# Performance work log

Measured on AMD Instinct MI355X. Metric: run time of the kernel, lower is better.

The kernel has to match this reference:

```python
import jax, jax.numpy as jnp
import numpy as np
from jax.ops import segment_sum

N_NODES = 100000
IN_CH = 128
HIDDEN = 256
N_EDGES = 1600000


def setup_inputs() -> dict:
    key = jax.random.key(0)
    ks = jax.random.split(key, 8)
    x = jax.random.normal(ks[0], (N_NODES, IN_CH), dtype=jnp.float32)
    edge_index = jax.random.randint(ks[1], (2, N_EDGES), 0, N_NODES, dtype=jnp.int64)
    edges = jax.random.randint(ks[2], (N_EDGES, 2), 0, N_NODES, dtype=jnp.int64)
    s1 = 1.0 / np.sqrt(IN_CH)
    s2 = 1.0 / np.sqrt(HIDDEN)
    W1l = jax.random.normal(ks[3], (IN_CH, HIDDEN), dtype=jnp.float32) * s1
    W1r = jax.random.normal(ks[4], (IN_CH, HIDDEN), dtype=jnp.float32) * s1
    b1 = jnp.zeros((HIDDEN,), dtype=jnp.float32)
    W2l = jax.random.normal(ks[5], (HIDDEN, HIDDEN), dtype=jnp.float32) * s2
    W2r = jax.random.normal(ks[6], (HIDDEN, HIDDEN), dtype=jnp.float32) * s2
    b2 = jnp.zeros((HIDDEN,), dtype=jnp.float32)
    return {"x": x, "edge_index": edge_index, "edges": edges,
            "W1l": W1l, "b1": b1, "W1r": W1r,
            "W2l": W2l, "b2": b2, "W2r": W2r}


def _sage_conv(x, src, dst, Wl, b, Wr, n_nodes):
    # PyG SAGEConv (aggr='mean'): out = lin_l(mean_{j in N(i)} x_j) + lin_r(x_i)
    msg_sum = segment_sum(x[src], dst, num_segments=n_nodes)        # [N, F]
    deg = segment_sum(jnp.ones((src.shape[0],), x.dtype), dst, num_segments=n_nodes)
    mean = msg_sum / jnp.maximum(deg, 1.0)[:, None]                 # zero-deg -> 0
    return mean @ Wl + b + x @ Wr


def reference(x, edge_index, edges, W1l, b1, W1r, W2l, b2, W2r):
    src, dst = edge_index[0], edge_index[1]
    n = x.shape[0]
    h = jax.nn.relu(_sage_conv(x, src, dst, W1l, b1, W1r, n))
    z = _sage_conv(h, src, dst, W2l, b2, W2r, n)                    # [N, hidden]
    # decode: dot product over candidate edge pairs
    return jnp.sum(z[edges[:, 0]] * z[edges[:, 1]], axis=-1)        # [E2]
```

## Files before the change

### kernel.cpp

```cpp
#include <hip/hip_runtime.h>

#define IN_CH 128
#define HID   256
#define PB_VT 16
#define BCAP  6144

typedef __attribute__((ext_vector_type(8))) short bf16x8;
typedef __attribute__((ext_vector_type(4))) float f32x4;
typedef __attribute__((ext_vector_type(2))) float f32x2;
typedef __attribute__((ext_vector_type(8))) unsigned short ushort8;

__device__ __forceinline__ ushort f2b(float f) {
    unsigned u = __float_as_uint(f);
    unsigned r = (u + 0x7fffu + ((u >> 16) & 1u)) >> 16;
    return (ushort)r;
}
__device__ __forceinline__ float b2f(ushort h) {
    return __uint_as_float(((unsigned)h) << 16);
}
__device__ __forceinline__ void fp8x8_to_f32(uint2 v, float f[8]) {
    f32x2 a = __builtin_amdgcn_cvt_pk_f32_fp8((int)v.x, false);
    f32x2 b = __builtin_amdgcn_cvt_pk_f32_fp8((int)v.x, true);
    f32x2 c = __builtin_amdgcn_cvt_pk_f32_fp8((int)v.y, false);
    f32x2 d = __builtin_amdgcn_cvt_pk_f32_fp8((int)v.y, true);
    f[0] = a[0]; f[1] = a[1]; f[2] = b[0]; f[3] = b[1];
    f[4] = c[0]; f[5] = c[1]; f[6] = d[0]; f[7] = d[1];
}

__device__ __forceinline__ void prep_w_body(const float* __restrict__ Wl,
                                            const float* __restrict__ Wr,
                                            ushort* __restrict__ Wt,
                                            int KH, bool permK, int idx) {
    int ktot = 2 * KH;
    if (idx >= 256 * ktot) return;
    int n = idx / ktot, k = idx % ktot;
    int kh = (k < KH) ? k : (k - KH);
    int c = kh;
    if (permK) {
        int j = kh & 63;
        c = (kh & ~63) | ((j & 3) * 16 + (j >> 2));
    }
    float v = (k < KH) ? Wl[(size_t)c * 256 + n] : Wr[(size_t)c * 256 + n];
    Wt[idx] = f2b(v);
}

__global__ __launch_bounds__(256)
void fused_cvt_prep(const float* __restrict__ x, ushort* __restrict__ xb, int n4, int nCvt,
                    const float* __restrict__ W1l, const float* __restrict__ W1r, ushort* __restrict__ Wt1,
                    const float* __restrict__ W2l, const float* __restrict__ W2r, ushort* __restrict__ Wt2,
                    int* __restrict__ bucketCntG, int* __restrict__ bucketCntP) {
    int b = blockIdx.x;
    int t = threadIdx.x;
    if (b < nCvt) {
        int i = b * 256 + t;
        if (i < n4) {
            float4 v = ((const float4*)x)[i];
            ushort4 u;
            u.x = f2b(v.x); u.y = f2b(v.y); u.z = f2b(v.z); u.w = f2b(v.w);
            ((ushort4*)xb)[i] = u;
        }
    } else if (b < nCvt + 256) {
        prep_w_body(W1l, W1r, Wt1, IN_CH, false, (b - nCvt) * 256 + t);
    } else if (b < nCvt + 256 + 512) {
        prep_w_body(W2l, W2r, Wt2, HID, true, (b - nCvt - 256) * 256 + t);
    } else {
        bucketCntG[t] = 0;
        bucketCntG[t + 256] = 0;
        bucketCntP[t] = 0;
        bucketCntP[t + 256] = 0;
    }
}

__global__ __launch_bounds__(256)
void scatter_reserve_kernel(const int* __restrict__ src, const int* __restrict__ dst,
                            const int* __restrict__ edges,
                            int* __restrict__ bucketCntG, int* __restrict__ bucketCntP,
                            unsigned* __restrict__ tmpG, unsigned long long* __restrict__ tmpP,
                            int E, int E2, int NBUK, int NBG) {
    __shared__ int hist[512];
    __shared__ int cur[512];
    int t = threadIdx.x;
    bool isG = (int)blockIdx.x < NBG;
    int blk = isG ? blockIdx.x : blockIdx.x - NBG;
    for (int i = t; i < NBUK; i += 256) hist[i] = 0;
    __syncthreads();
    long long e0 = (long long)blk * (256 * PB_VT);
    if (isG) {
#pragma unroll
        for (int i = 0; i < PB_VT; i++) {
            long long e = e0 + i * 256 + t;
            if (e < E) atomicAdd(&hist[dst[e] >> 8], 1);
        }
    } else {
#pragma unroll
        for (int i = 0; i < PB_VT; i++) {
            long long e = e0 + i * 256 + t;
            if (e < E2) atomicAdd(&hist[edges[e * 2] >> 8], 1);
        }
    }
    __syncthreads();
    int* bcnt = isG ? bucketCntG : bucketCntP;
    for (int i = t; i < NBUK; i += 256) {
        int hc = hist[i];
        cur[i] = (hc > 0) ? atomicAdd(&bcnt[i], hc) : 0;
    }
    __syncthreads();
    if (isG) {
#pragma unroll
        for (int i = 0; i < PB_VT; i++) {
            long long e = e0 + i * 256 + t;
            if (e < E) {
                int d = dst[e];
                int bk = d >> 8;
                int pos = atomicAdd(&cur[bk], 1);
                tmpG[(size_t)bk * BCAP + pos] = ((unsigned)src[e] << 8) | (unsigned)(d & 255);
            }
        }
    } else {
#pragma unroll
        for (int i = 0; i < PB_VT; i++) {
            long long e = e0 + i * 256 + t;
            if (e < E2) {
                int2 ab = *(const int2*)(edges + e * 2);
                int bk = ab.x >> 8;
                int pos = atomicAdd(&cur[bk], 1);
                tmpP[(size_t)bk * BCAP + pos] = ((unsigned long long)(unsigned)(ab.x & 255) << 56)
                                              | ((unsigned long long)(unsigned)ab.y << 32)
                                              | (unsigned)e;
            }
        }
    }
}

__global__ __launch_bounds__(256)
void bucket_sort_kernel(const unsigned* __restrict__ tmpG, const unsigned long long* __restrict__ tmpP,
                        const int* __restrict__ bucketCntG, const int* __restrict__ bucketCntP,
                        int* __restrict__ count, int* __restrict__ offs,
                        int* __restrict__ nbr, unsigned long long* __restrict__ pairs,
                        int N, int Npad, int NBUK) {
    __shared__ int h[256], loffs[256], lcur[256];
    int t = threadIdx.x;
    bool isG = (int)blockIdx.x < NBUK;
    int b = isG ? blockIdx.x : blockIdx.x - NBUK;
    int s = b * BCAP;
    int c = isG ? bucketCntG[b] : bucketCntP[b];
    h[t] = 0;
    __syncthreads();
    if (isG) {
        for (int i = t; i < c; i += 256) atomicAdd(&h[tmpG[s + i] & 255], 1);
    } else {
        for (int i = t; i < c; i += 256) atomicAdd(&h[(int)(tmpP[s + i] >> 56)], 1);
    }
    __syncthreads();
    int v = h[t];
    loffs[t] = v;
    __syncthreads();
    for (int d = 1; d < 256; d <<= 1) {
        int u = (t >= d) ? loffs[t - d] : 0;
        __syncthreads(); loffs[t] += u; __syncthreads();
    }
    int excl = loffs[t] - v;
    lcur[t] = excl;
    int node = b * 256 + t;
    if (node < N) {
        int base = isG ? 0 : Npad;
        count[base + node] = v;
        offs[base + node] = s + excl;
    }
    __syncthreads();
    if (isG) {
        for (int i = t; i < c; i += 256) {
            unsigned w = tmpG[s + i];
            int p = atomicAdd(&lcur[w & 255], 1);
            nbr[s + p] = (int)(w >> 8);
        }
    } else {
        for (int i = t; i < c; i += 256) {
            unsigned long long w = tmpP[s + i];
            int p = atomicAdd(&lcur[(int)(w >> 56)], 1);
            pairs[s + p] = w & 0x00FFFFFFFFFFFFFFull;
        }
    }
}

__global__ void agg1_kernel(const ushort* __restrict__ xb, const int* __restrict__ nbr,
                            const int* __restrict__ offs, const int* __restrict__ count,
                            ushort* __restrict__ agg, int N) {
    int w = blockIdx.x * 4 + (threadIdx.x >> 6);
    if (w >= N) return;
    int lane = threadIdx.x & 63;
    int grp = lane >> 4, gl = lane & 15;
    int start = offs[w], cnt = count[w];
    float a0[8], a1[8];
#pragma unroll
    for (int i = 0; i < 8; i++) { a0[i] = 0.0f; a1[i] = 0.0f; }
    int j = grp;
    for (; j + 4 < cnt; j += 8) {
        int s0 = nbr[start + j];
        int s1 = nbr[start + j + 4];
        ushort8 v0 = *(const ushort8*)(xb + (size_t)s0 * IN_CH + gl * 8);
        ushort8 v1 = *(const ushort8*)(xb + (size_t)s1 * IN_CH + gl * 8);
#pragma unroll
        for (int i = 0; i < 8; i++) { a0[i] += b2f(v0[i]); a1[i] += b2f(v1[i]); }
    }
    if (j < cnt) {
        int s0 = nbr[start + j];
        ushort8 v0 = *(const ushort8*)(xb + (size_t)s0 * IN_CH + gl * 8);
#pragma unroll
        for (int i = 0; i < 8; i++) a0[i] += b2f(v0[i]);
    }
#pragma unroll
    for (int i = 0; i < 8; i++) {
        a0[i] += a1[i];
        a0[i] += __shfl_xor(a0[i], 16, 64);
        a0[i] += __shfl_xor(a0[i], 32, 64);
    }
    if (grp == 0) {
        float r = 1.0f / fmaxf((float)cnt, 1.0f);
        ushort8 o;
#pragma unroll
        for (int i = 0; i < 8; i++) o[i] = f2b(a0[i] * r);
        *(ushort8*)(agg + (size_t)w * IN_CH + gl * 8) = o;
    }
}

__global__ void agg2_kernel(const unsigned char* __restrict__ h8, const int* __restrict__ nbr,
                            const int* __restrict__ offs, const int* __restrict__ count,
                            ushort* __restrict__ agg, int N) {
    int w = blockIdx.x * 4 + (threadIdx.x >> 6);
    if (w >= N) return;
    int lane = threadIdx.x & 63;
    int half = lane >> 5, hl = lane & 31;
    int start = offs[w], cnt = count[w];
    float a0[8], a1[8];
#pragma unroll
    for (int i = 0; i < 8; i++) { a0[i] = 0.0f; a1[i] = 0.0f; }
    int j = half;
    for (; j + 6 < cnt; j += 8) {
        int s0 = nbr[start + j];
        int s1 = nbr[start + j + 2];
        int s2 = nbr[start + j + 4];
        int s3 = nbr[start + j + 6];
        uint2 v0 = *(const uint2*)(h8 + (size_t)s0 * HID + hl * 8);
        uint2 v1 = *(const uint2*)(h8 + (size_t)s1 * HID + hl * 8);
        uint2 v2 = *(const uint2*)(h8 + (size_t)s2 * HID + hl * 8);
        uint2 v3 = *(const uint2*)(h8 + (size_t)s3 * HID + hl * 8);
        float f0[8], f1[8], f2[8], f3[8];
        fp8x8_to_f32(v0, f0); fp8x8_to_f32(v1, f1);
        fp8x8_to_f32(v2, f2); fp8x8_to_f32(v3, f3);
#pragma unroll
        for (int i = 0; i < 8; i++) {
            a0[i] += f0[i] + f2[i];
            a1[i] += f1[i] + f3[i];
        }
    }
    for (; j < cnt; j += 2) {
        int s0 = nbr[start + j];
        uint2 v0 = *(const uint2*)(h8 + (size_t)s0 * HID + hl * 8);
        float f0[8];
        fp8x8_to_f32(v0, f0);
#pragma unroll
        for (int i = 0; i < 8; i++) a0[i] += f0[i];
    }
#pragma unroll
    for (int i = 0; i < 8; i++) {
        a0[i] += a1[i];
        a0[i] += __shfl_xor(a0[i], 32, 64);
    }
    if (half == 0) {
        float r = 1.0f / fmaxf((float)cnt, 1.0f);
        ushort8 o;
#pragma unroll
        for (int i = 0; i < 8; i++) o[i] = f2b(a0[i] * r);
        *(ushort8*)(agg + (size_t)w * HID + hl * 8) = o;
    }
}

template<int KTOT, bool RELU, bool WBF16, bool WFP8>
__global__ __launch_bounds__(512, 4)
void sage_gemm_mfma(const ushort* __restrict__ Aleft, const ushort* __restrict__ Aright,
                    const ushort* __restrict__ Wt, const float* __restrict__ bias,
                    ushort* __restrict__ out, unsigned char* __restrict__ out8, int N) {
    constexpr int KH = KTOT / 2;
    __shared__ ushort smem[2048 + 8192];
    ushort* As = smem;
    ushort* Bs = smem + 2048;

    const int t = threadIdx.x;
    const int wave = t >> 6;
    const int lane = t & 63;
    const int quad = lane >> 4;
    const int l16  = lane & 15;
    const int rowBase = blockIdx.x * 64;

    const int aRow = t >> 3;
    const int aK   = (t & 7) * 4;
    const bool aRowOK = (rowBase + aRow) < N;
    const int aLds = ((aRow >> 4) * 64 + (aRow & 15) * 4 + (aK >> 3)) * 8 + (aK & 7);

    const int bN   = t >> 1;
    const int bCh0 = (t & 1) * 2;
    const int bFragBase = (bN >> 6) * 256 + ((bN >> 4) & 3) * 64 + (bN & 15) * 4;

    int bFrag[2];
#pragma unroll
    for (int nt = 0; nt < 2; nt++) {
        int c = wave * 32 + nt * 16 + l16;
        bFrag[nt] = ((c >> 6) * 256 + ((c >> 4) & 3) * 64 + (c & 15) * 4 + quad) * 8;
    }

    f32x4 acc[4][2];
#pragma unroll
    for (int i = 0; i < 4; i++)
#pragma unroll
        for (int j = 0; j < 2; j++) acc[i][j] = (f32x4)0.0f;

    unsigned long long aReg = 0ull;
    ulonglong2 bReg[2];
    if (aRowOK)
        aReg = *(const unsigned long long*)(Aleft + (size_t)(rowBase + aRow) * KH + aK);
    bReg[0] = *(const ulonglong2*)(Wt + (size_t)bN * KTOT + bCh0 * 8);
    bReg[1] = *(const ulonglong2*)(Wt + (size_t)bN * KTOT + (bCh0 + 1) * 8);

    for (int k0 = 0; k0 < KTOT; k0 += 32) {
        __syncthreads();
        *(unsigned long long*)&As[aLds] = aReg;
        *(ulonglong2*)&Bs[(bFragBase + bCh0) * 8]     = bReg[0];
        *(ulonglong2*)&Bs[(bFragBase + bCh0 + 1) * 8] = bReg[1];

        int kn = k0 + 32;
        if (kn < KTOT) {
            if (aRowOK) {
                const ushort* Ap = (kn < KH)
                    ? (Aleft  + (size_t)(rowBase + aRow) * KH + (kn + aK))
                    : (Aright + (size_t)(rowBase + aRow) * KH + (kn - KH + aK));
                aReg = *(const unsigned long long*)Ap;
            }
            bReg[0] = *(const ulonglong2*)(Wt + (size_t)bN * KTOT + kn + bCh0 * 8);
            bReg[1] = *(const ulonglong2*)(Wt + (size_t)bN * KTOT + kn + (bCh0 + 1) * 8);
        }
        __syncthreads();

        bf16x8 af[4], bf[2];
#pragma unroll
        for (int mt = 0; mt < 4; mt++)
            af[mt] = *(const bf16x8*)&As[(mt * 64 + l16 * 4 + quad) * 8];
#pragma unroll
        for (int nt = 0; nt < 2; nt++)
            bf[nt] = *(const bf16x8*)&Bs[bFrag[nt]];
#pragma unroll
        for (int mt = 0; mt < 4; mt++)
#pragma unroll
            for (int nt = 0; nt < 2; nt++)
                acc[mt][nt] = __builtin_amdgcn_mfma_f32_16x16x32_bf16(
                    af[mt], bf[nt], acc[mt][nt], 0, 0, 0);
    }

    float bv[2];
#pragma unroll
    for (int nt = 0; nt < 2; nt++) bv[nt] = bias[wave * 32 + nt * 16 + l16];
    ushort* tile = smem;

#pragma unroll
    for (int hf = 0; hf < 2; hf++) {
        __syncthreads();
#pragma unroll
        for (int mh = 0; mh < 2; mh++) {
            int mt = hf * 2 + mh;
#pragma unroll
            for (int reg = 0; reg < 4; reg++) {
                int rl = mh * 16 + quad * 4 + reg;
                float v0 = acc[mt][0][reg] + bv[0];
                float v1 = acc[mt][1][reg] + bv[1];
                if (RELU) { v0 = fmaxf(v0, 0.0f); v1 = fmaxf(v1, 0.0f); }
                ushort2 o;
                o.x = f2b(v0); o.y = f2b(v1);
                *(ushort2*)&tile[rl * 256 + (wave >> 1) * 64 + l16 * 4 + (wave & 1) * 2] = o;
            }
        }
        __syncthreads();
#pragma unroll
        for (int i = 0; i < 2; i++) {
            int ch = i * 512 + t;
            int rl = ch >> 5, c16 = ch & 31;
            int row = rowBase + hf * 32 + rl;
            if (row < N) {
                ushort8 w = *(const ushort8*)&tile[rl * 256 + c16 * 8];
                if (WBF16)
                    *(ushort8*)(out + (size_t)row * 256 + c16 * 8) = w;
                if (WFP8) {
                    int u0 = __builtin_amdgcn_cvt_pk_fp8_f32(b2f(w[0]), b2f(w[1]), 0, false);
                    u0 = __builtin_amdgcn_cvt_pk_fp8_f32(b2f(w[2]), b2f(w[3]), u0, true);
                    int u1 = __builtin_amdgcn_cvt_pk_fp8_f32(b2f(w[4]), b2f(w[5]), 0, false);
                    u1 = __builtin_amdgcn_cvt_pk_fp8_f32(b2f(w[6]), b2f(w[7]), u1, true);
                    uint2 o8;
                    o8.x = (unsigned)u0; o8.y = (unsigned)u1;
                    *(uint2*)(out8 + (size_t)row * 256 + c16 * 8) = o8;
                }
            }
        }
    }
}

__global__ void decode2_kernel(const unsigned char* __restrict__ z8,
                               const unsigned long long* __restrict__ pairs,
                               const int* __restrict__ offsA, const int* __restrict__ countA,
                               float* __restrict__ out, int N) {
    int a = blockIdx.x * 4 + (threadIdx.x >> 6);
    if (a >= N) return;
    int cnt = countA[a];
    if (cnt == 0) return;
    int lane = threadIdx.x & 63;
    int half = lane >> 5, hl = lane & 31;
    int start = offsA[a];

    float ar[8];
    {
        uint2 va = *(const uint2*)(z8 + (size_t)a * HID + hl * 8);
        fp8x8_to_f32(va, ar);
    }

    int j = half;
    for (; j + 6 < cnt; j += 8) {
        unsigned long long p0 = pairs[start + j];
        unsigned long long p1 = pairs[start + j + 2];
        unsigned long long p2 = pairs[start + j + 4];
        unsigned long long p3 = pairs[start + j + 6];
        int b0 = (int)((p0 >> 32) & 0xFFFFFFu), e0 = (int)(p0 & 0xffffffffu);
        int b1 = (int)((p1 >> 32) & 0xFFFFFFu), e1 = (int)(p1 & 0xffffffffu);
        int b2 = (int)((p2 >> 32) & 0xFFFFFFu), e2 = (int)(p2 & 0xffffffffu);
        int b3 = (int)((p3 >> 32) & 0xFFFFFFu), e3 = (int)(p3 & 0xffffffffu);
        uint2 v0 = *(const uint2*)(z8 + (size_t)b0 * HID + hl * 8);
        uint2 v1 = *(const uint2*)(z8 + (size_t)b1 * HID + hl * 8);
        uint2 v2 = *(const uint2*)(z8 + (size_t)b2 * HID + hl * 8);
        uint2 v3 = *(const uint2*)(z8 + (size_t)b3 * HID + hl * 8);
        float f0[8], f1[8], f2[8], f3[8];
        fp8x8_to_f32(v0, f0); fp8x8_to_f32(v1, f1);
        fp8x8_to_f32(v2, f2); fp8x8_to_f32(v3, f3);
        float s0 = 0.f, s1 = 0.f, s2 = 0.f, s3 = 0.f;
#pragma unroll
        for (int i = 0; i < 8; i++) {
            s0 = fmaf(ar[i], f0[i], s0);
            s1 = fmaf(ar[i], f1[i], s1);
            s2 = fmaf(ar[i], f2[i], s2);
            s3 = fmaf(ar[i], f3[i], s3);
        }
#pragma unroll
        for (int off = 1; off < 32; off <<= 1) {
            s0 += __shfl_xor(s0, off, 64);
            s1 += __shfl_xor(s1, off, 64);
            s2 += __shfl_xor(s2, off, 64);
            s3 += __shfl_xor(s3, off, 64);
        }
        if (hl == 0) { out[e0] = s0; out[e1] = s1; out[e2] = s2; out[e3] = s3; }
    }
    for (; j < cnt; j += 2) {
        unsigned long long p0 = pairs[start + j];
        int b0 = (int)((p0 >> 32) & 0xFFFFFFu), e0 = (int)(p0 & 0xffffffffu);
        uint2 v0 = *(const uint2*)(z8 + (size_t)b0 * HID + hl * 8);
        float f0[8];
        fp8x8_to_f32(v0, f0);
        float s0 = 0.f;
#pragma unroll
        for (int i = 0; i < 8; i++) s0 = fmaf(ar[i], f0[i], s0);
#pragma unroll
        for (int off = 1; off < 32; off <<= 1) s0 += __shfl_xor(s0, off, 64);
        if (hl == 0) out[e0] = s0;
    }
}

extern "C" void kernel_launch(void* const* d_in, const int* in_sizes, int n_in,
                              void* d_out, int out_size, void* d_ws, size_t ws_size,
                              hipStream_t stream) {
    const float* x    = (const float*)d_in[0];
    const int* eidx   = (const int*)d_in[1];
    const int* edges  = (const int*)d_in[2];
    const float* W1l  = (const float*)d_in[3];
    const float* b1   = (const float*)d_in[4];
    const float* W1r  = (const float*)d_in[5];
    const float* W2l  = (const float*)d_in[6];
    const float* b2   = (const float*)d_in[7];
    const float* W2r  = (const float*)d_in[8];
    float* out = (float*)d_out;

    const int N  = in_sizes[0] / IN_CH;
    const int E  = in_sizes[1] / 2;
    const int E2 = in_sizes[2] / 2;
    const int* src = eidx;
    const int* dst = eidx + E;

    const int NBUK = (N + 255) >> 8;
    const int Npad = NBUK << 8;
    const int NBG  = (E  + 256 * PB_VT - 1) / (256 * PB_VT);
    const int NBP  = (E2 + 256 * PB_VT - 1) / (256 * PB_VT);

    int* count      = (int*)d_ws;
    int* offs       = count + 2 * Npad;
    int* bucketCntG = offs + 2 * Npad;
    int* bucketCntP = bucketCntG + 512;
    int* nbr        = bucketCntP + 512;
    size_t intWords = (size_t)(nbr - (int*)d_ws) + (size_t)NBUK * BCAP;
    intWords = (intWords + 1) & ~(size_t)1;
    unsigned long long* pairs = (unsigned long long*)((int*)d_ws + intWords);
    ushort* xb    = (ushort*)(pairs + (size_t)NBUK * BCAP);
    ushort* agg1b = xb + (size_t)N * IN_CH;
    ushort* agg2b = xb;
    ushort* h     = agg1b + (size_t)N * IN_CH;
    unsigned char* h8 = (unsigned char*)(h + (size_t)N * HID);
    unsigned char* z8 = h8 + (size_t)N * HID;
    ushort* Wt1   = (ushort*)(z8 + (size_t)N * HID);
    ushort* Wt2   = Wt1 + 256 * 256;
    unsigned* tmpG = (unsigned*)h8;
    unsigned long long* tmpP =
        (unsigned long long*)(tmpG + (((size_t)NBUK * BCAP + 1) & ~(size_t)1));

    int n4 = N * IN_CH / 4;
    int nCvt = (n4 + 255) / 256;
    fused_cvt_prep<<<nCvt + 256 + 512 + 1, 256, 0, stream>>>(
        x, xb, n4, nCvt, W1l, W1r, Wt1, W2l, W2r, Wt2, bucketCntG, bucketCntP);

    scatter_reserve_kernel<<<NBG + NBP, 256, 0, stream>>>(
        src, dst, edges, bucketCntG, bucketCntP, tmpG, tmpP, E, E2, NBUK, NBG);
    bucket_sort_kernel<<<2 * NBUK, 256, 0, stream>>>(
        tmpG, tmpP, bucketCntG, bucketCntP, count, offs, nbr, pairs, N, Npad, NBUK);

    agg1_kernel<<<(N + 3) / 4, 256, 0, stream>>>(xb, nbr, offs, count, agg1b, N);
    sage_gemm_mfma<2 * IN_CH, true, true, true><<<(N + 63) / 64, 512, 0, stream>>>(
        agg1b, xb, Wt1, b1, h, h8, N);

    agg2_kernel<<<(N + 3) / 4, 256, 0, stream>>>(h8, nbr, offs, count, agg2b, N);
    sage_gemm_mfma<2 * HID, false, false, true><<<(N + 63) / 64, 512, 0, stream>>>(
        agg2b, h, Wt2, b2, h , z8, N);

    decode2_kernel<<<(N + 3) / 4, 256, 0, stream>>>(z8, pairs, offs + Npad, count + Npad, out, N);
}
```

Before: 539.7 us.

## Fuse front-end prep with bucket scatter and gather FP8 features in agg1

Merges the conversion/weight-prep kernel and the bucket scatter/reserve kernel into a single launch, replacing the counter zeroing with a memset. The input conversion now also writes an FP8 copy of x, which the first aggregation gathers instead of bf16, halving the bytes read per neighbor. This removes a kernel launch and its serialization and cuts gather bandwidth. The cost is lower precision in the layer-1 mean aggregation. The x8 buffer is placed at z8 plus N*HID/2 and may overlap z8 data, though z8 is written later.

```diff
diff --git a/kernel.cpp b/kernel.cpp
--- a/kernel.cpp
+++ b/kernel.cpp
@@ -45,10 +45,17 @@
 }
 
 __global__ __launch_bounds__(256)
-void fused_cvt_prep(const float* __restrict__ x, ushort* __restrict__ xb, int n4, int nCvt,
-                    const float* __restrict__ W1l, const float* __restrict__ W1r, ushort* __restrict__ Wt1,
-                    const float* __restrict__ W2l, const float* __restrict__ W2r, ushort* __restrict__ Wt2,
-                    int* __restrict__ bucketCntG, int* __restrict__ bucketCntP) {
+void fused_front(const float* __restrict__ x, ushort* __restrict__ xb,
+                 unsigned char* __restrict__ x8, int n4, int nCvt,
+                 const float* __restrict__ W1l, const float* __restrict__ W1r, ushort* __restrict__ Wt1,
+                 const float* __restrict__ W2l, const float* __restrict__ W2r, ushort* __restrict__ Wt2,
+                 const int* __restrict__ src, const int* __restrict__ dst,
+                 const int* __restrict__ edges,
+                 int* __restrict__ bucketCntG, int* __restrict__ bucketCntP,
+                 unsigned* __restrict__ tmpG, unsigned long long* __restrict__ tmpP,
+                 int E, int E2, int NBUK, int NBG) {
+    __shared__ int hist[512];
+    __shared__ int cur[512];
     int b = blockIdx.x;
     int t = threadIdx.x;
     if (b < nCvt) {
@@ -58,30 +65,18 @@
             ushort4 u;
             u.x = f2b(v.x); u.y = f2b(v.y); u.z = f2b(v.z); u.w = f2b(v.w);
             ((ushort4*)xb)[i] = u;
-        }
-    } else if (b < nCvt + 256) {
-        prep_w_body(W1l, W1r, Wt1, IN_CH, false, (b - nCvt) * 256 + t);
-    } else if (b < nCvt + 256 + 512) {
-        prep_w_body(W2l, W2r, Wt2, HID, true, (b - nCvt - 256) * 256 + t);
-    } else {
-        bucketCntG[t] = 0;
-        bucketCntG[t + 256] = 0;
-        bucketCntP[t] = 0;
-        bucketCntP[t + 256] = 0;
-    }
-}
-
-__global__ __launch_bounds__(256)
-void scatter_reserve_kernel(const int* __restrict__ src, const int* __restrict__ dst,
-                            const int* __restrict__ edges,
-                            int* __restrict__ bucketCntG, int* __restrict__ bucketCntP,
-                            unsigned* __restrict__ tmpG, unsigned long long* __restrict__ tmpP,
-                            int E, int E2, int NBUK, int NBG) {
-    __shared__ int hist[512];
-    __shared__ int cur[512];
-    int t = threadIdx.x;
-    bool isG = (int)blockIdx.x < NBG;
-    int blk = isG ? blockIdx.x : blockIdx.x - NBG;
+            int p = __builtin_amdgcn_cvt_pk_fp8_f32(v.x, v.y, 0, false);
+            p = __builtin_amdgcn_cvt_pk_fp8_f32(v.z, v.w, p, true);
+            ((unsigned*)x8)[i] = (unsigned)p;
+        }
+        return;
+    }
+    if (b < nCvt + 256) { prep_w_body(W1l, W1r, Wt1, IN_CH, false, (b - nCvt) * 256 + t); return; }
+    if (b < nCvt + 768) { prep_w_body(W2l, W2r, Wt2, HID, true, (b - nCvt - 256) * 256 + t); return; }
+
+    int vb = b - (nCvt + 768);
+    bool isG = vb < NBG;
+    int blk = isG ? vb : vb - NBG;
     for (int i = t; i < NBUK; i += 256) hist[i] = 0;
     __syncthreads();
     long long e0 = (long long)blk * (256 * PB_VT);
@@ -183,7 +178,7 @@
     }
 }
 
-__global__ void agg1_kernel(const ushort* __restrict__ xb, const int* __restrict__ nbr,
+__global__ void agg1_kernel(const unsigned char* __restrict__ x8, const int* __restrict__ nbr,
                             const int* __restrict__ offs, const int* __restrict__ count,
                             ushort* __restrict__ agg, int N) {
     int w = blockIdx.x * 4 + (threadIdx.x >> 6);
@@ -198,16 +193,20 @@
     for (; j + 4 < cnt; j += 8) {
         int s0 = nbr[start + j];
         int s1 = nbr[start + j + 4];
-        ushort8 v0 = *(const ushort8*)(xb + (size_t)s0 * IN_CH + gl * 8);
-        ushort8 v1 = *(const ushort8*)(xb + (size_t)s1 * IN_CH + gl * 8);
-#pragma unroll
-        for (int i = 0; i < 8; i++) { a0[i] += b2f(v0[i]); a1[i] += b2f(v1[i]); }
+        uint2 v0 = *(const uint2*)(x8 + (size_t)s0 * IN_CH + gl * 8);
+        uint2 v1 = *(const uint2*)(x8 + (size_t)s1 * IN_CH + gl * 8);
+        float f0[8], f1[8];
+        fp8x8_to_f32(v0, f0); fp8x8_to_f32(v1, f1);
+#pragma unroll
+        for (int i = 0; i < 8; i++) { a0[i] += f0[i]; a1[i] += f1[i]; }
     }
     if (j < cnt) {
         int s0 = nbr[start + j];
-        ushort8 v0 = *(const ushort8*)(xb + (size_t)s0 * IN_CH + gl * 8);
-#pragma unroll
-        for (int i = 0; i < 8; i++) a0[i] += b2f(v0[i]);
+        uint2 v0 = *(const uint2*)(x8 + (size_t)s0 * IN_CH + gl * 8);
+        float f0[8];
+        fp8x8_to_f32(v0, f0);
+#pragma unroll
+        for (int i = 0; i < 8; i++) a0[i] += f0[i];
     }
 #pragma unroll
     for (int i = 0; i < 8; i++) {
@@ -510,21 +509,23 @@
     unsigned char* z8 = h8 + (size_t)N * HID;
     ushort* Wt1   = (ushort*)(z8 + (size_t)N * HID);
     ushort* Wt2   = Wt1 + 256 * 256;
+    unsigned char* x8 = z8 + (size_t)N * HID / 2;
     unsigned* tmpG = (unsigned*)h8;
     unsigned long long* tmpP =
         (unsigned long long*)(tmpG + (((size_t)NBUK * BCAP + 1) & ~(size_t)1));
 
+    hipMemsetAsync(bucketCntG, 0, 1024 * sizeof(int), stream);
+
     int n4 = N * IN_CH / 4;
     int nCvt = (n4 + 255) / 256;
-    fused_cvt_prep<<<nCvt + 256 + 512 + 1, 256, 0, stream>>>(
-        x, xb, n4, nCvt, W1l, W1r, Wt1, W2l, W2r, Wt2, bucketCntG, bucketCntP);
-
-    scatter_reserve_kernel<<<NBG + NBP, 256, 0, stream>>>(
+    fused_front<<<nCvt + 768 + NBG + NBP, 256, 0, stream>>>(
+        x, xb, x8, n4, nCvt, W1l, W1r, Wt1, W2l, W2r, Wt2,
         src, dst, edges, bucketCntG, bucketCntP, tmpG, tmpP, E, E2, NBUK, NBG);
+
     bucket_sort_kernel<<<2 * NBUK, 256, 0, stream>>>(
         tmpG, tmpP, bucketCntG, bucketCntP, count, offs, nbr, pairs, N, Npad, NBUK);
 
-    agg1_kernel<<<(N + 3) / 4, 256, 0, stream>>>(xb, nbr, offs, count, agg1b, N);
+    agg1_kernel<<<(N + 3) / 4, 256, 0, stream>>>(x8, nbr, offs, count, agg1b, N);
     sage_gemm_mfma<2 * IN_CH, true, true, true><<<(N + 63) / 64, 512, 0, stream>>>(
         agg1b, xb, Wt1, b1, h, h8, N);
 
```

After: 559.6 us. 3.7% more time.
